# Performance work log

Measured on AMD Instinct MI355X. Metric: run time of the kernel, lower is better.

## Reference

```python
import jax, jax.numpy as jnp
import numpy as np

B, T, C, H = 2, 2048, 1024, 16
HD = C // H  # 64
EPS = 1e-5


def _ln(x, g, b):
    mu = jnp.mean(x, axis=-1, keepdims=True)
    var = jnp.var(x, axis=-1, keepdims=True)
    return (x - mu) * jax.lax.rsqrt(var + EPS) * g + b


def setup_inputs() -> dict:
    key = jax.random.key(0)
    ks = jax.random.split(key, 8)
    s = lambda n: 1.0 / np.sqrt(n)
    return {
        "x": jax.random.normal(ks[0], (B, T, C), dtype=jnp.float32),
        "ln1_g": jnp.ones((C,), jnp.float32), "ln1_b": jnp.zeros((C,), jnp.float32),
        "ln2_g": jnp.ones((C,), jnp.float32), "ln2_b": jnp.zeros((C,), jnp.float32),
        "w_in": jax.random.normal(ks[1], (C, 3 * C), jnp.float32) * s(C),
        "b_in": jnp.zeros((3 * C,), jnp.float32),
        "w_out": jax.random.normal(ks[2], (C, C), jnp.float32) * s(C),
        "b_out": jnp.zeros((C,), jnp.float32),
        "w_fc": jax.random.normal(ks[3], (C, 4 * C), jnp.float32) * s(C),
        "b_fc": jnp.zeros((4 * C,), jnp.float32),
        "w_proj": jax.random.normal(ks[4], (4 * C, C), jnp.float32) * s(4 * C),
        "b_proj": jnp.zeros((C,), jnp.float32),
    }


def reference(x, ln1_g, ln1_b, ln2_g, ln2_b, w_in, b_in, w_out, b_out,
              w_fc, b_fc, w_proj, b_proj):
    # --- residual 1: x + attn(ln1(x)) ---
    h = _ln(x, ln1_g, ln1_b)
    qkv = h @ w_in + b_in                          # (B,T,3C)
    # reshape to (B,T,H,3*HD) then chunk per head (matches torch code exactly)
    qkv = qkv.reshape(B, T, H, 3 * HD).transpose(0, 2, 1, 3)  # (B,H,T,3*HD)
    q, k, v = jnp.split(qkv, 3, axis=-1)           # each (B,H,T,HD)
    att = jnp.einsum('bhqd,bhkd->bhqk', q, k) / np.sqrt(HD)
    causal = jnp.tril(jnp.ones((T, T), bool))
    att = jnp.where(causal, att, -jnp.inf)
    att = jax.nn.softmax(att, axis=-1)
    o = jnp.einsum('bhqk,bhkd->bhqd', att, v)      # (B,H,T,HD)
    o = o.transpose(0, 2, 1, 3).reshape(B, T, C)
    x1 = x + (o @ w_out + b_out)
    # --- ln2 applied to residual stream, then residual 2 on top of ln2 output ---
    y = _ln(x1, ln2_g, ln2_b)
    mlp = jax.nn.gelu(y @ w_fc + b_fc, approximate=False) @ w_proj + b_proj
    return y + mlp
```

## Files before the change

### kernel.cpp

```cpp
#include <hip/hip_runtime.h>
#include <hip/hip_bf16.h>
#include <math.h>

typedef __bf16 bf16;
typedef __bf16 bf16x8 __attribute__((ext_vector_type(8)));
typedef __bf16 bf16x4 __attribute__((ext_vector_type(4)));
typedef float floatx4 __attribute__((ext_vector_type(4)));
typedef int intx4 __attribute__((ext_vector_type(4)));

#define B_ 2
#define T_ 2048
#define C_ 1024
#define H_ 16
#define HD_ 64

__device__ __forceinline__ void gload_lds16(const bf16* g, bf16* l) {
    __builtin_amdgcn_global_load_lds(
        (const __attribute__((address_space(1))) unsigned int*)(g),
        (__attribute__((address_space(3))) unsigned int*)(l), 16, 0, 0);
}

__global__ __launch_bounds__(256) void transpose_all(
        const float* __restrict__ w_in, const float* __restrict__ w_out,
        const float* __restrict__ w_fc, const float* __restrict__ w_proj,
        bf16* __restrict__ o_in, bf16* __restrict__ o_out,
        bf16* __restrict__ o_fc, bf16* __restrict__ o_proj) {
    __shared__ float shf[32 * 33];
    int t = blockIdx.x;
    int tid = threadIdx.x;
    const float* src; bf16* dst; int K, N, idx;
    if (t < 3072)      { src = w_in;   dst = o_in;   K = 1024; N = 3072; idx = t; }
    else if (t < 7168) { src = w_fc;   dst = o_fc;   K = 1024; N = 4096; idx = t - 3072; }
    else if (t < 8192) { src = w_out;  dst = o_out;  K = 1024; N = 1024; idx = t - 7168; }
    else               { src = w_proj; dst = o_proj; K = 4096; N = 1024; idx = t - 8192; }
    int ntx = N >> 5;
    int nt = (idx % ntx) * 32, kt = (idx / ntx) * 32;
    int tx = tid & 31, ty = tid >> 5;
    #pragma unroll
    for (int i = 0; i < 32; i += 8)
        shf[(ty + i) * 33 + tx] = src[(size_t)(kt + ty + i) * N + nt + tx];
    __syncthreads();
    #pragma unroll
    for (int i = 0; i < 32; i += 8)
        dst[(size_t)(nt + ty + i) * K + kt + tx] = (bf16)shf[tx * 33 + ty + i];
}

__global__ __launch_bounds__(256) void ln_kernel(const float* __restrict__ x,
                                                 const float* __restrict__ g,
                                                 const float* __restrict__ b,
                                                 bf16* __restrict__ out_b,
                                                 float* __restrict__ out_f) {
    int row = blockIdx.x;
    int tid = threadIdx.x;
    const float* xr = x + (size_t)row * C_;
    float4 v = ((const float4*)xr)[tid];
    float s  = v.x + v.y + v.z + v.w;
    float ss = v.x * v.x + v.y * v.y + v.z * v.z + v.w * v.w;
    #pragma unroll
    for (int off = 32; off; off >>= 1) {
        s  += __shfl_down(s, off);
        ss += __shfl_down(ss, off);
    }
    __shared__ float red[8];
    int wid = tid >> 6;
    if ((tid & 63) == 0) { red[wid] = s; red[wid + 4] = ss; }
    __syncthreads();
    s  = red[0] + red[1] + red[2] + red[3];
    ss = red[4] + red[5] + red[6] + red[7];
    float mean = s * (1.0f / C_);
    float var  = ss * (1.0f / C_) - mean * mean;
    float rstd = rsqrtf(var + 1e-5f);
    float4 gv = ((const float4*)g)[tid];
    float4 bv = ((const float4*)b)[tid];
    float o0 = (v.x - mean) * rstd * gv.x + bv.x;
    float o1 = (v.y - mean) * rstd * gv.y + bv.y;
    float o2 = (v.z - mean) * rstd * gv.z + bv.z;
    float o3 = (v.w - mean) * rstd * gv.w + bv.w;
    bf16x4 ob = { (bf16)o0, (bf16)o1, (bf16)o2, (bf16)o3 };
    ((bf16x4*)out_b)[(size_t)row * 256 + tid] = ob;
    if (out_f) {
        float4 of; of.x = o0; of.y = o1; of.z = o2; of.w = o3;
        ((float4*)out_f)[(size_t)row * 256 + tid] = of;
    }
}

__device__ __forceinline__ float gelu_fast(float x) {
    float z2 = 1.5957691216f * (x + 0.044715f * x * x * x);
    float e = __expf(z2);
    float t = 1.0f - 2.0f * __builtin_amdgcn_rcpf(e + 1.0f);
    return 0.5f * x * (1.0f + t);
}

#define BAR() do { __builtin_amdgcn_sched_barrier(0); __builtin_amdgcn_s_barrier(); __builtin_amdgcn_sched_barrier(0); } while (0)
#define VMC6() asm volatile("s_waitcnt vmcnt(6)" ::: "memory")
#define VMC0() asm volatile("s_waitcnt vmcnt(0)" ::: "memory")

#define LOAD_A(AS, QM) \
  { _Pragma("unroll") for (int i_ = 0; i_ < 4; i_++) { \
      const int r_ = wm128 + ((QM) * 4 + i_) * 16 + lm; \
      _Pragma("unroll") for (int kc_ = 0; kc_ < 2; kc_++) \
        aR[i_][kc_] = *(const bf16x8*)((AS) + r_ * 64 + ((((kc_ << 2) | quad) ^ (lm & 7)) << 3)); } }

#define LOAD_B(BS, QN) \
  { _Pragma("unroll") for (int j_ = 0; j_ < 2; j_++) { \
      const int r_ = wn64 + ((QN) * 2 + j_) * 16 + lm; \
      _Pragma("unroll") for (int kc_ = 0; kc_ < 2; kc_++) \
        bR[QN][j_][kc_] = *(const bf16x8*)((BS) + r_ * 64 + ((((kc_ << 2) | quad) ^ (lm & 7)) << 3)); } }

#define MFMA_Q(QM, QN) \
  { __builtin_amdgcn_s_setprio(1); \
    _Pragma("unroll") for (int i_ = 0; i_ < 4; i_++) \
    _Pragma("unroll") for (int j_ = 0; j_ < 2; j_++) \
    _Pragma("unroll") for (int kc_ = 0; kc_ < 2; kc_++) \
      acc[(QM) * 4 + i_][(QN) * 2 + j_] = __builtin_amdgcn_mfma_f32_16x16x32_bf16( \
          aR[i_][kc_], bR[QN][j_][kc_], acc[(QM) * 4 + i_][(QN) * 2 + j_], 0, 0, 0); \
    __builtin_amdgcn_s_setprio(0); }

#define STG(gb, lb, r0v, k0v) \
    gload_lds16((gb) + (size_t)((r0v) + sr8) * K + (k0v) + scb, (lb) + ((r0v) + wid * 8) * 64)

template<int MODE>
__global__ __launch_bounds__(512, 2) void gemm256(const bf16* __restrict__ A,
                                                  const bf16* __restrict__ Bt,
                                                  const float* __restrict__ bias,
                                                  void* __restrict__ out,
                                                  int M, int N, int K) {
    (void)M;
    __shared__ __align__(16) bf16 smem[4 * 256 * 64];
    bf16* As0 = smem;
    bf16* Bs0 = smem + 1 * 256 * 64;
    bf16* As1 = smem + 2 * 256 * 64;
    bf16* Bs1 = smem + 3 * 256 * 64;

    int ntn = N >> 8;
    int lin = blockIdx.x;
    int x = lin & 7, local = lin >> 3;
    int RN = (ntn == 12) ? 3 : 4;
    int rsz = 4 * RN;
    int r = local / rsz, s = local - r * rsz;
    int rid = x + 8 * r;
    int mt = (rid & 3) * 4 + (s & 3);
    int nt = (rid >> 2) * RN + (s >> 2);
    int m0 = mt << 8, n0 = nt << 8;

    int tid = threadIdx.x;
    int wid = __builtin_amdgcn_readfirstlane(tid >> 6);
    int lane = tid & 63;
    int lm = lane & 15, quad = lane >> 4;
    int wm128 = (wid & 1) * 128;
    int wn64  = (wid >> 1) * 64;

    const bf16* Ablk = A  + (size_t)m0 * K;
    const bf16* Bblk = Bt + (size_t)n0 * K;

    int sr8 = wid * 8 + (lane >> 3);
    int scb = ((lane & 7) ^ (lane >> 3)) << 3;

    floatx4 acc[8][4];
    #pragma unroll
    for (int f = 0; f < 8; f++)
        #pragma unroll
        for (int g = 0; g < 4; g++) { floatx4 z = {0.f, 0.f, 0.f, 0.f}; acc[f][g] = z; }
    bf16x8 aR[4][2], bR[2][2][2];

    int nI = K >> 7;

    STG(Ablk, As0, 0, 0);   STG(Ablk, As0, 64, 0);
    STG(Ablk, As0, 128, 0); STG(Ablk, As0, 192, 0);
    STG(Bblk, Bs0, 0, 0);   STG(Bblk, Bs0, 64, 0);
    STG(Bblk, Bs0, 128, 0); STG(Bblk, Bs0, 192, 0);
    STG(Ablk, As1, 0, 64);  STG(Ablk, As1, 128, 64);
    STG(Bblk, Bs1, 0, 64);  STG(Bblk, Bs1, 64, 64);
    STG(Ablk, As1, 64, 64); STG(Ablk, As1, 192, 64);
    VMC6();
    BAR();

    for (int it = 0; it < nI; it++) {
        int kE = (2 * it + 2) << 6;
        int kO = (2 * it + 3) << 6;
        int kT = (2 * it + 1) << 6;
        bool nl = (it + 1 < nI);
        LOAD_A(As0, 0); LOAD_B(Bs0, 0);
        STG(Bblk, Bs1, 128, kT); STG(Bblk, Bs1, 192, kT);
        BAR(); MFMA_Q(0, 0); BAR();
        LOAD_B(Bs0, 1);
        if (nl) { STG(Ablk, As0, 0, kE); STG(Ablk, As0, 128, kE); }
        BAR(); MFMA_Q(0, 1); BAR();
        LOAD_A(As0, 1);
        if (nl) { STG(Bblk, Bs0, 0, kE); STG(Bblk, Bs0, 64, kE); }
        BAR(); MFMA_Q(1, 0); BAR();
        if (nl) { STG(Ablk, As0, 64, kE); STG(Ablk, As0, 192, kE); }
        BAR(); MFMA_Q(1, 1);
        if (nl) { VMC6(); } else { VMC0(); }
        BAR();
        LOAD_A(As1, 0); LOAD_B(Bs1, 0);
        if (nl) { STG(Bblk, Bs0, 128, kE); STG(Bblk, Bs0, 192, kE); }
        BAR(); MFMA_Q(0, 0); BAR();
        LOAD_B(Bs1, 1);
        if (nl) { STG(Ablk, As1, 0, kO); STG(Ablk, As1, 128, kO); }
        BAR(); MFMA_Q(0, 1); BAR();
        LOAD_A(As1, 1);
        if (nl) { STG(Bblk, Bs1, 0, kO); STG(Bblk, Bs1, 64, kO); }
        BAR(); MFMA_Q(1, 0); BAR();
        if (nl) { STG(Ablk, As1, 64, kO); STG(Ablk, As1, 192, kO); }
        BAR(); MFMA_Q(1, 1);
        if (nl) { VMC6(); }
        BAR();
    }

    bf16* ob = (bf16*)out;
    bf16* patch = smem + wid * (64 * 68);
    #pragma unroll
    for (int h = 0; h < 2; h++) {
        #pragma unroll
        for (int ff = 0; ff < 4; ff++)
            #pragma unroll
            for (int g = 0; g < 4; g++) {
                int n = n0 + wn64 + g * 16 + lm;
                float bsn = bias[n];
                #pragma unroll
                for (int r2 = 0; r2 < 4; r2++) {
                    float v = acc[h * 4 + ff][g][r2] + bsn;
                    if (MODE == 1) v = gelu_fast(v);
                    patch[(ff * 16 + quad * 4 + r2) * 68 + g * 16 + lm] = (bf16)v;
                }
            }
        #pragma unroll
        for (int ff = 0; ff < 4; ff++)
            #pragma unroll
            for (int kc = 0; kc < 2; kc++) {
                bf16x8 v = *(const bf16x8*)&patch[(ff * 16 + lm) * 68 + kc * 32 + quad * 8];
                size_t row = (size_t)(m0 + wm128 + h * 64 + ff * 16 + lm);
                *(bf16x8*)(ob + row * N + n0 + wn64 + kc * 32 + quad * 8) = v;
            }
    }
}

#define VMCP(n) asm volatile("s_waitcnt vmcnt(" #n ")" ::: "memory")

#define STGP(kt) { bf16* bs_ = smem + ((kt) & 3) * 16384; \
    gload_lds16(Ab + (size_t)sr8 * K + (kt) * 64 + scb,        bs_ + (wid * 8) * 64); \
    gload_lds16(Ab + (size_t)(64 + sr8) * K + (kt) * 64 + scb, bs_ + (64 + wid * 8) * 64); \
    gload_lds16(Bb + (size_t)sr8 * K + (kt) * 64 + scb,        bs_ + 8192 + (wid * 8) * 64); \
    gload_lds16(Bb + (size_t)(64 + sr8) * K + (kt) * 64 + scb, bs_ + 8192 + (64 + wid * 8) * 64); }

__global__ __launch_bounds__(512, 2) void gemm_npipe(const bf16* __restrict__ A,
                                                     const bf16* __restrict__ Bt,
                                                     const float* __restrict__ bias,
                                                     const float* __restrict__ add,
                                                     float* __restrict__ out,
                                                     int N, int K) {
    __shared__ __align__(16) bf16 smem[4 * 16384];
    int lin = blockIdx.x;
    int x = lin & 7, local = lin >> 3;
    int r = local >> 2, s = local & 3;
    int rid = x + 8 * r;
    int m0 = ((rid & 15) * 2 + (s & 1)) * 128;
    int n0 = ((rid >> 4) * 2 + (s >> 1)) * 128;
    int tid = threadIdx.x;
    int wid = __builtin_amdgcn_readfirstlane(tid >> 6);
    int lane = tid & 63;
    int lm = lane & 15, quad = lane >> 4;
    int wm32 = (wid & 3) * 32, wn64 = (wid >> 2) * 64;
    int sr8 = wid * 8 + (lane >> 3);
    int scb = ((lane & 7) ^ (lane >> 3)) << 3;
    const bf16* Ab = A  + (size_t)m0 * K;
    const bf16* Bb = Bt + (size_t)n0 * K;
    int NT = K >> 6;

    floatx4 acc[2][4];
    #pragma unroll
    for (int i = 0; i < 2; i++)
        #pragma unroll
        for (int j = 0; j < 4; j++) { floatx4 z = {0.f, 0.f, 0.f, 0.f}; acc[i][j] = z; }
    bf16x8 aR[2][2], bR[4][2];

    STGP(0); STGP(1); STGP(2);
    VMCP(8);
    BAR();

    for (int t = 0; t < NT; t++) {
        if (t + 3 < NT) STGP(t + 3);
        bf16* bs = smem + (t & 3) * 16384;
        #pragma unroll
        for (int i = 0; i < 2; i++)
            #pragma unroll
            for (int kc = 0; kc < 2; kc++)
                aR[i][kc] = *(const bf16x8*)(bs + (wm32 + i * 16 + lm) * 64 +
                                             ((((kc << 2) | quad) ^ (lm & 7)) << 3));
        #pragma unroll
        for (int j = 0; j < 4; j++)
            #pragma unroll
            for (int kc = 0; kc < 2; kc++)
                bR[j][kc] = *(const bf16x8*)(bs + 8192 + (wn64 + j * 16 + lm) * 64 +
                                             ((((kc << 2) | quad) ^ (lm & 7)) << 3));
        __builtin_amdgcn_s_setprio(1);
        #pragma unroll
        for (int kc = 0; kc < 2; kc++)
            #pragma unroll
            for (int i = 0; i < 2; i++)
                #pragma unroll
                for (int j = 0; j < 4; j++)
                    acc[i][j] = __builtin_amdgcn_mfma_f32_16x16x32_bf16(
                        aR[i][kc], bR[j][kc], acc[i][j], 0, 0, 0);
        __builtin_amdgcn_s_setprio(0);
        if (t + 3 < NT)      { VMCP(8); }
        else if (t == NT - 3){ VMCP(4); }
        else if (t == NT - 2){ VMCP(0); }
        BAR();
    }

    #pragma unroll
    for (int i = 0; i < 2; i++)
        #pragma unroll
        for (int j = 0; j < 4; j++) {
            int mbase = m0 + wm32 + i * 16 + quad * 4;
            int n     = n0 + wn64 + j * 16 + lm;
            float bsn = bias[n];
            #pragma unroll
            for (int r2 = 0; r2 < 4; r2++) {
                size_t idx = (size_t)(mbase + r2) * N + n;
                out[idx] = acc[i][j][r2] + bsn + add[idx];
            }
        }
}

#define QT_ 128
#define KT_ 64

__device__ __forceinline__ void vt_stage(bf16* VtB, bf16x8 vv, int vdb,
                                         int vcolb, int oddf) {
    intx4 vi = *(intx4*)&vv;
    intx4 pi;
    #pragma unroll
    for (int m = 0; m < 4; m++) pi[m] = __shfl_xor(vi[m], 8);
    #pragma unroll
    for (int j = 0; j < 4; j++) {
        int w0 = j >> 1, sh = (j & 1) * 16;
        unsigned int oe = ((unsigned int)vi[w0] >> sh) & 0xffffu;
        unsigned int pe = ((unsigned int)pi[w0] >> sh) & 0xffffu;
        unsigned int oo = ((unsigned int)vi[2 + w0] >> sh) & 0xffffu;
        unsigned int po = ((unsigned int)pi[2 + w0] >> sh) & 0xffffu;
        unsigned int de = oe | (pe << 16);
        unsigned int dn = po | (oo << 16);
        unsigned int dw = oddf ? dn : de;
        *(unsigned int*)(VtB + (size_t)(vdb + j) * 72 + vcolb) = dw;
    }
}

__global__ __launch_bounds__(512) void attn_mfma_kernel(const bf16* __restrict__ qkv,
                                                        bf16* __restrict__ Opart,
                                                        float* __restrict__ mlw) {
    int bh = blockIdx.x;
    int b = bh >> 4, h = bh & 15;
    int cy = blockIdx.y;
    int y, ci;
    if (cy < 4)       { y = cy;                   ci = 0; }
    else if (cy < 12) { y = 4 + ((cy - 4) >> 1);  ci = (cy - 4) & 1; }
    else if (cy < 24) { y = 8 + (cy - 12) / 3;    ci = (cy - 12) % 3; }
    else              { y = 12 + ((cy - 24) >> 2); ci = (cy - 24) & 3; }
    int q0 = y * QT_;
    int tb = ci * 8;
    int te = 2 * y + 2; if (te > tb + 8) te = tb + 8;

    int tid = threadIdx.x;
    int wid = __builtin_amdgcn_readfirstlane(tid >> 6);
    int lane = tid & 63;
    int lm = lane & 15, quad = lane >> 4;
    int sw = lm & 7;
    int r0 = q0 + wid * 16;

    const bf16* base = qkv + (size_t)b * T_ * (3 * C_) + h * (3 * HD_);

    __shared__ __align__(16) bf16 Ks[2][KT_][64];
    __shared__ __align__(16) bf16 Vt[2][HD_][72];
    __shared__ __align__(16) bf16 PsT[8][16][64];

    bf16x8 qf[2];
    #pragma unroll
    for (int kc = 0; kc < 2; kc++) {
        bf16x8 t = *(const bf16x8*)(base + (size_t)(r0 + lm) * (3 * C_) + kc * 32 + quad * 8);
        #pragma unroll
        for (int e = 0; e < 8; e++) t[e] = (bf16)((float)t[e] * 0.1803368801f);
        qf[kc] = t;
    }

    floatx4 acc_o[4];
    #pragma unroll
    for (int dn = 0; dn < 4; dn++) { floatx4 z = {0.f, 0.f, 0.f, 0.f}; acc_o[dn] = z; }
    float mst = -1e30f, lst = 0.0f;

    int srow = tid >> 3;
    int scb  = ((lane & 7) ^ (lane >> 3)) << 3;
    int scol = (tid & 7) * 8;
    int oddf = srow & 1;
    int vcolb = (((srow >> 3) ^ (tid & 7)) << 3) + (srow & 6);
    int vdb   = scol + (oddf ? 4 : 0);

    {
        size_t gr = (size_t)(tb * KT_ + srow) * (3 * C_);
        gload_lds16(base + gr + HD_ + scb, &Ks[0][wid * 8][0]);
        bf16x8 vv = *(const bf16x8*)(base + gr + 2 * HD_ + scol);
        vt_stage(&Vt[0][0][0], vv, vdb, vcolb, oddf);
        __syncthreads();
    }

    for (int t = tb; t < te; t++) {
        int cur = t & 1;
        bool pre = (t + 1 < te);
        bf16x8 vv;
        if (pre) {
            size_t nrow = (size_t)((t + 1) * KT_ + srow) * (3 * C_);
            gload_lds16(base + nrow + HD_ + scb, &Ks[cur ^ 1][wid * 8][0]);
            vv = *(const bf16x8*)(base + nrow + 2 * HD_ + scol);
        }
        __builtin_amdgcn_sched_barrier(0);

        int k0 = t * KT_;
        if (k0 <= r0 + 15) {
            floatx4 st[4];
            #pragma unroll
            for (int bn = 0; bn < 4; bn++) { floatx4 z = {0.f, 0.f, 0.f, 0.f}; st[bn] = z; }
            #pragma unroll
            for (int kc = 0; kc < 2; kc++) {
                bf16x8 kf[4];
                #pragma unroll
                for (int bn = 0; bn < 4; bn++)
                    kf[bn] = *(const bf16x8*)(&Ks[cur][bn * 16 + lm]
                                              [((((kc << 2) | quad) ^ sw) << 3)]);
                __builtin_amdgcn_s_setprio(1);
                #pragma unroll
                for (int bn = 0; bn < 4; bn++)
                    st[bn] = __builtin_amdgcn_mfma_f32_16x16x32_bf16(kf[bn], qf[kc], st[bn], 0, 0, 0);
                __builtin_amdgcn_s_setprio(0);
            }

            float vv_[4][4];
            float rm = -1e30f;
            if (k0 + KT_ - 1 > r0) {
                int gq = r0 + lm;
                #pragma unroll
                for (int bn = 0; bn < 4; bn++) {
                    #pragma unroll
                    for (int r2 = 0; r2 < 4; r2++) {
                        int key = k0 + bn * 16 + quad * 4 + r2;
                        vv_[bn][r2] = (key <= gq) ? st[bn][r2] : -1e30f;
                    }
                    rm = fmaxf(rm, fmaxf(fmaxf(vv_[bn][0], vv_[bn][1]),
                                         fmaxf(vv_[bn][2], vv_[bn][3])));
                }
            } else {
                #pragma unroll
                for (int bn = 0; bn < 4; bn++) {
                    #pragma unroll
                    for (int r2 = 0; r2 < 4; r2++) vv_[bn][r2] = st[bn][r2];
                    rm = fmaxf(rm, fmaxf(fmaxf(vv_[bn][0], vv_[bn][1]),
                                         fmaxf(vv_[bn][2], vv_[bn][3])));
                }
            }
            rm = fmaxf(rm, __shfl_xor(rm, 16));
            rm = fmaxf(rm, __shfl_xor(rm, 32));
            float mnew = fmaxf(mst, rm);
            float alpha = exp2f(mst - mnew);
            mst = mnew;
            float ps = 0.f;
            #pragma unroll
            for (int bn = 0; bn < 4; bn++) {
                float p0 = exp2f(vv_[bn][0] - mnew);
                float p1 = exp2f(vv_[bn][1] - mnew);
                float p2 = exp2f(vv_[bn][2] - mnew);
                float p3 = exp2f(vv_[bn][3] - mnew);
                ps += (p0 + p1) + (p2 + p3);
                bf16x4 pk = { (bf16)p0, (bf16)p1, (bf16)p2, (bf16)p3 };
                int kb = bn * 2 + (quad >> 1);
                int col = ((kb ^ sw) << 3) + (quad & 1) * 4;
                *(bf16x4*)(&PsT[wid][lm][col]) = pk;
            }
            ps += __shfl_xor(ps, 16);
            ps += __shfl_xor(ps, 32);
            lst = lst * alpha + ps;

            #pragma unroll
            for (int r2 = 0; r2 < 4; r2++) {
                float ar = __shfl(alpha, quad * 4 + r2);
                #pragma unroll
                for (int dn = 0; dn < 4; dn++) acc_o[dn][r2] *= ar;
            }

            __asm__ volatile("s_waitcnt lgkmcnt(0)" ::: "memory");

            #pragma unroll
            for (int kc = 0; kc < 2; kc++) {
                bf16x8 pa = *(const bf16x8*)(&PsT[wid][lm][((kc * 4 + quad) ^ sw) << 3]);
                bf16x8 vfr[4];
                #pragma unroll
                for (int dn = 0; dn < 4; dn++) {
                    int d = dn * 16 + lm;
                    int swd = (d >> 3) & 7;
                    vfr[dn] = *(const bf16x8*)(&Vt[cur][d][(((kc * 4 + quad) ^ swd) << 3)]);
                }
                __builtin_amdgcn_s_setprio(1);
                #pragma unroll
                for (int dn = 0; dn < 4; dn++)
                    acc_o[dn] = __builtin_amdgcn_mfma_f32_16x16x32_bf16(pa, vfr[dn], acc_o[dn], 0, 0, 0);
                __builtin_amdgcn_s_setprio(0);
            }
        }

        if (pre) vt_stage(&Vt[cur ^ 1][0][0], vv, vdb, vcolb, oddf);
        __syncthreads();
    }

    #pragma unroll
    for (int r2 = 0; r2 < 4; r2++) {
        #pragma unroll
        for (int dn = 0; dn < 4; dn++)
            PsT[wid][quad * 4 + r2][dn * 16 + lm] = (bf16)acc_o[dn][r2];
    }
    __asm__ volatile("s_waitcnt lgkmcnt(0)" ::: "memory");
    bf16* op = Opart + ((size_t)bh * 40 + cy) * (QT_ * HD_) + (wid * 16 + lm) * HD_;
    #pragma unroll
    for (int kcl = 0; kcl < 2; kcl++) {
        bf16x8 v = *(const bf16x8*)&PsT[wid][lm][kcl * 32 + quad * 8];
        *(bf16x8*)(op + kcl * 32 + quad * 8) = v;
    }
    if (lane < 16) {
        float* mlp = mlw + (((size_t)bh * 40 + cy) * QT_ + wid * 16 + lane) * 2;
        mlp[0] = mst;
        mlp[1] = lst;
    }
}

__global__ __launch_bounds__(256) void attn_combine(const bf16* __restrict__ Opart,
                                                    const float* __restrict__ mlw,
                                                    bf16* __restrict__ ob) {
    int bh = blockIdx.x, y = blockIdx.y;
    int b = bh >> 4, h = bh & 15;
    int nc = (y >> 2) + 1;
    int cy0 = (y < 4) ? y : (y < 8) ? (4 + ((y - 4) << 1))
             : (y < 12) ? (12 + (y - 8) * 3) : (24 + ((y - 12) << 2));
    int tid = threadIdx.x;
    int row = tid >> 1, half = tid & 1;
    size_t cbase = (size_t)bh * 40 + cy0;
    const float* mlp = mlw + (cbase * QT_ + row) * 2;
    float m0 = mlp[0], l0 = mlp[1];
    float m1 = -1e30f, l1 = 0.f, m2 = -1e30f, l2 = 0.f, m3 = -1e30f, l3 = 0.f;
    if (nc > 1) { m1 = mlp[2 * QT_];     l1 = mlp[2 * QT_ + 1]; }
    if (nc > 2) { m2 = mlp[2 * 2 * QT_]; l2 = mlp[2 * 2 * QT_ + 1]; }
    if (nc > 3) { m3 = mlp[3 * 2 * QT_]; l3 = mlp[3 * 2 * QT_ + 1]; }
    float mx = fmaxf(fmaxf(m0, m1), fmaxf(m2, m3));
    float s0 = exp2f(m0 - mx), s1 = exp2f(m1 - mx);
    float s2 = exp2f(m2 - mx), s3 = exp2f(m3 - mx);
    float wsum = s0 * l0 + s1 * l1 + s2 * l2 + s3 * l3;

    const bf16* op = Opart + cbase * (QT_ * HD_) + row * HD_ + half * 32;
    float acc[32];
    #pragma unroll
    for (int v8 = 0; v8 < 4; v8++) {
        bf16x8 v = *(const bf16x8*)(op + v8 * 8);
        #pragma unroll
        for (int e = 0; e < 8; e++) acc[v8 * 8 + e] = s0 * (float)v[e];
    }
    if (nc > 1) {
        #pragma unroll
        for (int v8 = 0; v8 < 4; v8++) {
            bf16x8 v = *(const bf16x8*)(op + QT_ * HD_ + v8 * 8);
            #pragma unroll
            for (int e = 0; e < 8; e++) acc[v8 * 8 + e] += s1 * (float)v[e];
        }
    }
    if (nc > 2) {
        #pragma unroll
        for (int v8 = 0; v8 < 4; v8++) {
            bf16x8 v = *(const bf16x8*)(op + 2 * QT_ * HD_ + v8 * 8);
            #pragma unroll
            for (int e = 0; e < 8; e++) acc[v8 * 8 + e] += s2 * (float)v[e];
        }
    }
    if (nc > 3) {
        #pragma unroll
        for (int v8 = 0; v8 < 4; v8++) {
            bf16x8 v = *(const bf16x8*)(op + 3 * QT_ * HD_ + v8 * 8);
            #pragma unroll
            for (int e = 0; e < 8; e++) acc[v8 * 8 + e] += s3 * (float)v[e];
        }
    }
    float inv = 1.0f / wsum;
    bf16* dst = ob + ((size_t)(b * T_ + y * QT_ + row)) * C_ + h * HD_ + half * 32;
    #pragma unroll
    for (int v8 = 0; v8 < 4; v8++) {
        bf16x8 o;
        #pragma unroll
        for (int e = 0; e < 8; e++) o[e] = (bf16)(acc[v8 * 8 + e] * inv);
        *(bf16x8*)(dst + v8 * 8) = o;
    }
}

extern "C" void kernel_launch(void* const* d_in, const int* in_sizes, int n_in,
                              void* d_out, int out_size, void* d_ws, size_t ws_size,
                              hipStream_t stream) {
    (void)in_sizes; (void)n_in; (void)out_size; (void)ws_size;
    const float* x      = (const float*)d_in[0];
    const float* ln1_g  = (const float*)d_in[1];
    const float* ln1_b  = (const float*)d_in[2];
    const float* ln2_g  = (const float*)d_in[3];
    const float* ln2_b  = (const float*)d_in[4];
    const float* w_in   = (const float*)d_in[5];
    const float* b_in   = (const float*)d_in[6];
    const float* w_out  = (const float*)d_in[7];
    const float* b_out  = (const float*)d_in[8];
    const float* w_fc   = (const float*)d_in[9];
    const float* b_fc   = (const float*)d_in[10];
    const float* w_proj = (const float*)d_in[11];
    const float* b_proj = (const float*)d_in[12];

    char* ws = (char*)d_ws;
    const size_t MB = 1024 * 1024;
    bf16*  w_inT   = (bf16*)(ws + 0);
    bf16*  w_outT  = (bf16*)(ws + 6 * MB);
    bf16*  w_fcT   = (bf16*)(ws + 8 * MB);
    bf16*  w_projT = (bf16*)(ws + 16 * MB);
    bf16*  qkv     = (bf16*)(ws + 24 * MB);
    bf16*  fc_b    = (bf16*)(ws + 24 * MB);
    bf16*  o_b     = (bf16*)(ws + 56 * MB);
    bf16*  y_b     = (bf16*)(ws + 56 * MB);
    bf16*  h_b     = (bf16*)(ws + 64 * MB);
    float* x1      = (float*)(ws + 64 * MB);
    float* y_f     = (float*)(ws + 80 * MB);
    bf16*  Opart   = (bf16*)(ws + 64 * MB);
    float* mlw     = (float*)(ws + 84 * MB);

    const int M = B_ * T_;

    transpose_all<<<12288, 256, 0, stream>>>(w_in, w_out, w_fc, w_proj,
                                             w_inT, w_outT, w_fcT, w_projT);

    ln_kernel<<<M, 256, 0, stream>>>(x, ln1_g, ln1_b, h_b, nullptr);
    gemm256<0><<<(M >> 8) * ((3 * C_) >> 8), 512, 0, stream>>>(h_b, w_inT, b_in,
                                                               qkv, M, 3 * C_, C_);
    attn_mfma_kernel<<<dim3(B_ * H_, 40), 512, 0, stream>>>(qkv, Opart, mlw);
    attn_combine<<<dim3(B_ * H_, T_ / QT_), 256, 0, stream>>>(Opart, mlw, o_b);
    gemm_npipe<<<256, 512, 0, stream>>>(o_b, w_outT, b_out, x, x1, C_, C_);
    ln_kernel<<<M, 256, 0, stream>>>(x1, ln2_g, ln2_b, y_b, y_f);
    gemm256<1><<<(M >> 8) * ((4 * C_) >> 8), 512, 0, stream>>>(y_b, w_fcT, b_fc,
                                                               fc_b, M, 4 * C_, C_);
    gemm_npipe<<<256, 512, 0, stream>>>(fc_b, w_projT, b_proj, y_f,
                                        (float*)d_out, C_, 4 * C_);
}
```

Measured before the change: 324.1 us.

## Move attention P fragments via lane shuffles, add lazy rescale and occupancy hint

The attention kernel no longer round-trips the softmax probabilities through shared memory. It packs them to bf16 pairs and rearranges them into MFMA A-operand layout with cross-lane shuffles, which removes the PsT buffer and an lgkmcnt wait. It also skips the running-max rescale of the output accumulator unless the new max exceeds the old one by more than 8 (log2 units), and adds a launch_bounds occupancy hint of 6 blocks. The GEMM macro is reordered so kc is the outer MFMA loop. Risks: extra register pressure from the shuffles, and unscaled exponentials up to 2^8 in bf16, which affects precision slightly.

```diff
diff --git a/kernel.cpp b/kernel.cpp
--- a/kernel.cpp
+++ b/kernel.cpp
@@ -7,6 +7,7 @@
 typedef __bf16 bf16x4 __attribute__((ext_vector_type(4)));
 typedef float floatx4 __attribute__((ext_vector_type(4)));
 typedef int intx4 __attribute__((ext_vector_type(4)));
+typedef unsigned int uintx4 __attribute__((ext_vector_type(4)));
 
 #define B_ 2
 #define T_ 2048
@@ -109,9 +110,9 @@
 
 #define MFMA_Q(QM, QN) \
   { __builtin_amdgcn_s_setprio(1); \
+    _Pragma("unroll") for (int kc_ = 0; kc_ < 2; kc_++) \
     _Pragma("unroll") for (int i_ = 0; i_ < 4; i_++) \
     _Pragma("unroll") for (int j_ = 0; j_ < 2; j_++) \
-    _Pragma("unroll") for (int kc_ = 0; kc_ < 2; kc_++) \
       acc[(QM) * 4 + i_][(QN) * 2 + j_] = __builtin_amdgcn_mfma_f32_16x16x32_bf16( \
           aR[i_][kc_], bR[QN][j_][kc_], acc[(QM) * 4 + i_][(QN) * 2 + j_], 0, 0, 0); \
     __builtin_amdgcn_s_setprio(0); }
@@ -328,6 +329,12 @@
 #define QT_ 128
 #define KT_ 64
 
+__device__ __forceinline__ unsigned int pk2(float a, float b) {
+    unsigned short ua = __builtin_bit_cast(unsigned short, (bf16)a);
+    unsigned short ub = __builtin_bit_cast(unsigned short, (bf16)b);
+    return (unsigned int)ua | ((unsigned int)ub << 16);
+}
+
 __device__ __forceinline__ void vt_stage(bf16* VtB, bf16x8 vv, int vdb,
                                          int vcolb, int oddf) {
     intx4 vi = *(intx4*)&vv;
@@ -348,9 +355,9 @@
     }
 }
 
-__global__ __launch_bounds__(512) void attn_mfma_kernel(const bf16* __restrict__ qkv,
-                                                        bf16* __restrict__ Opart,
-                                                        float* __restrict__ mlw) {
+__global__ __launch_bounds__(512, 6) void attn_mfma_kernel(const bf16* __restrict__ qkv,
+                                                           bf16* __restrict__ Opart,
+                                                           float* __restrict__ mlw) {
     int bh = blockIdx.x;
     int b = bh >> 4, h = bh & 15;
     int cy = blockIdx.y;
@@ -374,7 +381,6 @@
 
     __shared__ __align__(16) bf16 Ks[2][KT_][64];
     __shared__ __align__(16) bf16 Vt[2][HD_][72];
-    __shared__ __align__(16) bf16 PsT[8][16][64];
 
     bf16x8 qf[2];
     #pragma unroll
@@ -396,6 +402,10 @@
     int oddf = srow & 1;
     int vcolb = (((srow >> 3) ^ (tid & 7)) << 3) + (srow & 6);
     int vdb   = scol + (oddf ? 4 : 0);
+
+    int l01 = ((((quad & 1) << 1) | (quad >> 1)) << 4) + lm;
+    int l23 = l01 ^ 16;
+    bool hi = (quad & 2) != 0;
 
     {
         size_t gr = (size_t)(tb * KT_ + srow) * (3 * C_);
@@ -435,7 +445,6 @@
                 __builtin_amdgcn_s_setprio(0);
             }
 
-            float vv_[4][4];
             float rm = -1e30f;
             if (k0 + KT_ - 1 > r0) {
                 int gq = r0 + lm;
@@ -444,54 +453,71 @@
                     #pragma unroll
                     for (int r2 = 0; r2 < 4; r2++) {
                         int key = k0 + bn * 16 + quad * 4 + r2;
-                        vv_[bn][r2] = (key <= gq) ? st[bn][r2] : -1e30f;
+                        st[bn][r2] = (key <= gq) ? st[bn][r2] : -1e30f;
                     }
-                    rm = fmaxf(rm, fmaxf(fmaxf(vv_[bn][0], vv_[bn][1]),
-                                         fmaxf(vv_[bn][2], vv_[bn][3])));
+                    rm = fmaxf(rm, fmaxf(fmaxf(st[bn][0], st[bn][1]),
+                                         fmaxf(st[bn][2], st[bn][3])));
                 }
             } else {
                 #pragma unroll
-                for (int bn = 0; bn < 4; bn++) {
-                    #pragma unroll
-                    for (int r2 = 0; r2 < 4; r2++) vv_[bn][r2] = st[bn][r2];
-                    rm = fmaxf(rm, fmaxf(fmaxf(vv_[bn][0], vv_[bn][1]),
-                                         fmaxf(vv_[bn][2], vv_[bn][3])));
-                }
+                for (int bn = 0; bn < 4; bn++)
+                    rm = fmaxf(rm, fmaxf(fmaxf(st[bn][0], st[bn][1]),
+                                         fmaxf(st[bn][2], st[bn][3])));
             }
             rm = fmaxf(rm, __shfl_xor(rm, 16));
             rm = fmaxf(rm, __shfl_xor(rm, 32));
-            float mnew = fmaxf(mst, rm);
-            float alpha = exp2f(mst - mnew);
-            mst = mnew;
+
+            float mcur = mst;
+            if (!__all(rm <= mst + 8.0f)) {
+                float mnew = fmaxf(mst, rm);
+                float alpha = exp2f(mst - mnew);
+                lst *= alpha;
+                #pragma unroll
+                for (int r2 = 0; r2 < 4; r2++) {
+                    float ar = __shfl(alpha, quad * 4 + r2);
+                    #pragma unroll
+                    for (int dn = 0; dn < 4; dn++) acc_o[dn][r2] *= ar;
+                }
+                mst = mnew; mcur = mnew;
+            }
+
             float ps = 0.f;
+            unsigned int D01[4], D23[4];
             #pragma unroll
             for (int bn = 0; bn < 4; bn++) {
-                float p0 = exp2f(vv_[bn][0] - mnew);
-                float p1 = exp2f(vv_[bn][1] - mnew);
-                float p2 = exp2f(vv_[bn][2] - mnew);
-                float p3 = exp2f(vv_[bn][3] - mnew);
+                float p0 = exp2f(st[bn][0] - mcur);
+                float p1 = exp2f(st[bn][1] - mcur);
+                float p2 = exp2f(st[bn][2] - mcur);
+                float p3 = exp2f(st[bn][3] - mcur);
                 ps += (p0 + p1) + (p2 + p3);
-                bf16x4 pk = { (bf16)p0, (bf16)p1, (bf16)p2, (bf16)p3 };
-                int kb = bn * 2 + (quad >> 1);
-                int col = ((kb ^ sw) << 3) + (quad & 1) * 4;
-                *(bf16x4*)(&PsT[wid][lm][col]) = pk;
+                D01[bn] = pk2(p0, p1);
+                D23[bn] = pk2(p2, p3);
             }
             ps += __shfl_xor(ps, 16);
             ps += __shfl_xor(ps, 32);
-            lst = lst * alpha + ps;
-
-            #pragma unroll
-            for (int r2 = 0; r2 < 4; r2++) {
-                float ar = __shfl(alpha, quad * 4 + r2);
-                #pragma unroll
-                for (int dn = 0; dn < 4; dn++) acc_o[dn][r2] *= ar;
-            }
-
-            __asm__ volatile("s_waitcnt lgkmcnt(0)" ::: "memory");
-
+            lst += ps;
+
+            bf16x8 pa[2];
             #pragma unroll
             for (int kc = 0; kc < 2; kc++) {
-                bf16x8 pa = *(const bf16x8*)(&PsT[wid][lm][((kc * 4 + quad) ^ sw) << 3]);
+                unsigned int sA = (quad & 1) ? D01[kc * 2 + 1] : D01[kc * 2];
+                unsigned int sB = (quad & 1) ? D23[kc * 2 + 1] : D23[kc * 2];
+                unsigned int sC = (quad & 1) ? D01[kc * 2]     : D01[kc * 2 + 1];
+                unsigned int sD = (quad & 1) ? D23[kc * 2]     : D23[kc * 2 + 1];
+                unsigned int g0 = (unsigned int)__shfl((int)sA, l01);
+                unsigned int g1 = (unsigned int)__shfl((int)sB, l01);
+                unsigned int g2 = (unsigned int)__shfl((int)sC, l23);
+                unsigned int g3 = (unsigned int)__shfl((int)sD, l23);
+                uintx4 wv;
+                wv[0] = hi ? g2 : g0;
+                wv[1] = hi ? g3 : g1;
+                wv[2] = hi ? g0 : g2;
+                wv[3] = hi ? g1 : g3;
+                pa[kc] = __builtin_bit_cast(bf16x8, wv);
+            }
+
+            #pragma unroll
+            for (int kc = 0; kc < 2; kc++) {
                 bf16x8 vfr[4];
                 #pragma unroll
                 for (int dn = 0; dn < 4; dn++) {
@@ -502,7 +528,7 @@
                 __builtin_amdgcn_s_setprio(1);
                 #pragma unroll
                 for (int dn = 0; dn < 4; dn++)
-                    acc_o[dn] = __builtin_amdgcn_mfma_f32_16x16x32_bf16(pa, vfr[dn], acc_o[dn], 0, 0, 0);
+                    acc_o[dn] = __builtin_amdgcn_mfma_f32_16x16x32_bf16(pa[kc], vfr[dn], acc_o[dn], 0, 0, 0);
                 __builtin_amdgcn_s_setprio(0);
             }
         }
@@ -511,17 +537,18 @@
         __syncthreads();
     }
 
+    bf16* sc = &Ks[0][0][0] + wid * 1024;
     #pragma unroll
     for (int r2 = 0; r2 < 4; r2++) {
         #pragma unroll
         for (int dn = 0; dn < 4; dn++)
-            PsT[wid][quad * 4 + r2][dn * 16 + lm] = (bf16)acc_o[dn][r2];
+            sc[(quad * 4 + r2) * 64 + dn * 16 + lm] = (bf16)acc_o[dn][r2];
     }
     __asm__ volatile("s_waitcnt lgkmcnt(0)" ::: "memory");
     bf16* op = Opart + ((size_t)bh * 40 + cy) * (QT_ * HD_) + (wid * 16 + lm) * HD_;
     #pragma unroll
     for (int kcl = 0; kcl < 2; kcl++) {
-        bf16x8 v = *(const bf16x8*)&PsT[wid][lm][kcl * 32 + quad * 8];
+        bf16x8 v = *(const bf16x8*)&sc[lm * 64 + kcl * 32 + quad * 8];
         *(bf16x8*)(op + kcl * 32 + quad * 8) = v;
     }
     if (lane < 16) {
```

Result: slower. 345.4 us (+6.6%).
